# Optimization experiments

Measured on AMD Instinct MI355X. Metric: run time of the kernel, lower is better.

## Reference

```python
import jax, jax.numpy as jnp
import numpy as np

EPS = 1e-08


def setup_inputs() -> dict:
    key = jax.random.key(0)
    B, D = 8192, 512
    student_output = jax.random.normal(key, (B, D), dtype=jnp.float32)
    return {"student_output": student_output}


def reference(student_output) -> jnp.ndarray:
    # F.normalize(p=2, dim=-1, eps=EPS): x / max(||x||, eps)
    norm = jnp.linalg.norm(student_output, axis=-1, keepdims=True)
    x = student_output / jnp.maximum(norm, EPS)

    n = x.shape[0]
    # Pairwise inner products; mask the diagonal with -1 (self-match)
    dots = jnp.matmul(x, x.T)  # [B, B]
    idx = jnp.arange(n)
    dots = dots.at[idx, idx].set(-1.0)
    I = jnp.argmax(dots, axis=1)  # nearest neighbor index per row

    # torch.nn.PairwiseDistance(2, eps): ||x1 - x2 + eps||_2
    diff = x - x[I] + EPS
    distances = jnp.linalg.norm(diff, axis=-1)  # [B]
    loss = -jnp.mean(jnp.log(distances + EPS))
    return loss
```

## Files before the change

### kernel.cpp

```cpp
#include <hip/hip_runtime.h>
#include <hip/hip_bf16.h>
#include <math.h>

#define D_DIM 512
#define TM    128
#define TN    256

typedef int i32x4 __attribute__((ext_vector_type(4)));
typedef unsigned long long u64;


__device__ inline void async16(unsigned char* lds, const unsigned char* g) {
    __builtin_amdgcn_global_load_lds(
        (const __attribute__((address_space(1))) void*)g,
        (__attribute__((address_space(3))) void*)lds,
        16, 0, 0);
}


__global__ __launch_bounds__(256) void normalize_rows(
        const float* __restrict__ in, unsigned char* __restrict__ xb,
        float* __restrict__ inv_norm, u64* __restrict__ best,
        float* __restrict__ acc, int* __restrict__ cnt) {
    const int row  = blockIdx.x * 4 + (threadIdx.x >> 6);
    const int lane = threadIdx.x & 63;
    if (blockIdx.x == 0 && threadIdx.x == 0) { acc[0] = 0.f; cnt[0] = 0; }
    const float4* rp = (const float4*)(in + (size_t)row * D_DIM) + lane * 2;
    float4 a = rp[0], b = rp[1];
    float s = a.x*a.x + a.y*a.y + a.z*a.z + a.w*a.w
            + b.x*b.x + b.y*b.y + b.z*b.z + b.w*b.w;
    #pragma unroll
    for (int m = 1; m <= 32; m <<= 1) s += __shfl_xor(s, m, 64);
    float inv = 1.0f / fmaxf(sqrtf(s), 1e-8f);
    if (lane == 0) {
        inv_norm[row] = inv;
        best[row] = 0ull;
    }
    float sc = inv * 127.0f;
    int q0 = __float2int_rn(a.x*sc), q1 = __float2int_rn(a.y*sc);
    int q2 = __float2int_rn(a.z*sc), q3 = __float2int_rn(a.w*sc);
    int q4 = __float2int_rn(b.x*sc), q5 = __float2int_rn(b.y*sc);
    int q6 = __float2int_rn(b.z*sc), q7 = __float2int_rn(b.w*sc);
    int lo = (q0 & 255) | ((q1 & 255) << 8) | ((q2 & 255) << 16) | ((q3 & 255) << 24);
    int hi = (q4 & 255) | ((q5 & 255) << 8) | ((q6 & 255) << 16) | ((q7 & 255) << 24);
    ((int2*)(xb + (size_t)row * D_DIM))[lane] = make_int2(lo, hi);
}


__global__ __launch_bounds__(512, 4) void gemm_argmax(
        const unsigned char* __restrict__ X, u64* __restrict__ best) {
    __shared__ unsigned char smem[49152];
    unsigned char* As0 = smem;
    unsigned char* Bs0 = smem + 16384;
    unsigned int* rmerge = (unsigned int*)smem;
    unsigned int* cmerge = (unsigned int*)(smem + 2048);

    int l = blockIdx.x;
    int q = (int)(sqrtf((float)l / 16.0f + 0.25f) - 0.5f);
    while (16 * (q + 1) * (q + 2) <= l) ++q;
    while (16 * q * (q + 1) > l) --q;
    int rrem = l - 16 * q * (q + 1);
    int cw   = 8 * (q + 1);
    int c    = rrem / cw;
    int bi   = rrem - c * cw;
    int bj   = 4 * q + c;
    if (bi > 2 * bj + 1) return;
    const int m0 = bi * TM;
    const int n0 = bj * TN;

    const int t    = threadIdx.x;
    const int lane = t & 63;
    const int w    = t >> 6;
    const int wm   = w >> 2;
    const int wn   = w & 3;
    const int qr   = lane & 15;
    const int quad = lane >> 4;

    const int srcsl = ((t & 3) ^ ((t >> 3) & 3)) * 16;
    const unsigned char* gA  = X + (size_t)(m0 + (t >> 2)) * D_DIM + srcsl;
    const unsigned char* gB  = X + (size_t)(n0 + (t >> 2)) * D_DIM + srcsl;
    const unsigned char* gB2 = gB + (size_t)128 * D_DIM;

    #define STAGE(buf, k0)                                        \
        do {                                                      \
            async16(As0 + (buf) * 8192 + t * 16, gA + (k0));      \
            async16(Bs0 + (buf) * 16384 + t * 16, gB + (k0));     \
            async16(Bs0 + (buf) * 16384 + 8192 + t * 16, gB2 + (k0)); \
        } while (0)

    i32x4 accm[4][4];
    #pragma unroll
    for (int mi = 0; mi < 4; mi++)
        #pragma unroll
        for (int ni = 0; ni < 4; ni++)
            accm[mi][ni] = (i32x4){0, 0, 0, 0};

    const int rdsl = (quad ^ ((qr >> 1) & 3)) * 16;

    STAGE(0, 0);
    #pragma unroll
    for (int t8 = 0; t8 < 8; t8++) {
        const int cur = t8 & 1;
        if (t8 < 7) {
            STAGE(cur ^ 1, (t8 + 1) * 64);
            asm volatile("s_waitcnt vmcnt(3)" ::: "memory");
        } else {
            asm volatile("s_waitcnt vmcnt(0)" ::: "memory");
        }
        __builtin_amdgcn_s_barrier();

        i32x4 av[4], bv[4];
        const unsigned char* pA = As0 + cur * 8192  + (wm * 64 + qr) * 64 + rdsl;
        const unsigned char* pB = Bs0 + cur * 16384 + (wn * 64 + qr) * 64 + rdsl;
        #pragma unroll
        for (int mi = 0; mi < 4; mi++)
            av[mi] = *(const i32x4*)(pA + mi * 1024);
        #pragma unroll
        for (int ni = 0; ni < 4; ni++)
            bv[ni] = *(const i32x4*)(pB + ni * 1024);
        #pragma unroll
        for (int mi = 0; mi < 4; mi++)
            #pragma unroll
            for (int ni = 0; ni < 4; ni++)
                accm[mi][ni] = __builtin_amdgcn_mfma_i32_16x16x64_i8(
                    av[mi], bv[ni], accm[mi][ni], 0, 0, 0);

        asm volatile("" ::: "memory");
        __builtin_amdgcn_s_barrier();
    }
    #undef STAGE

    const int colg_base = n0 + wn * 64 + qr;

    #pragma unroll
    for (int mi = 0; mi < 4; mi++) {
        #pragma unroll
        for (int r = 0; r < 4; r++) {
            const int rowl = wm * 64 + mi * 16 + quad * 4 + r;
            const int rowg = m0 + rowl;
            unsigned key = 0u;
            #pragma unroll
            for (int ni = 0; ni < 4; ni++) {
                const int colg = colg_base + ni * 16;
                const unsigned lcol = (unsigned)(wn * 64 + ni * 16 + qr);
                unsigned k = (((unsigned)accm[mi][ni][r] + 0x800000u) << 8)
                           | (255u - lcol);
                k = (colg == rowg) ? 0u : k;
                key = key > k ? key : k;
            }
            #pragma unroll
            for (int m = 1; m <= 8; m <<= 1) {
                unsigned o = (unsigned)__shfl_xor((int)key, m, 64);
                key = key > o ? key : o;
            }
            if (qr == 0) rmerge[rowl * 4 + wn] = key;
        }
    }

    #pragma unroll
    for (int ni = 0; ni < 4; ni++) {
        const int colg = colg_base + ni * 16;
        unsigned key = 0u;
        #pragma unroll
        for (int mi = 0; mi < 4; mi++) {
            #pragma unroll
            for (int r = 0; r < 4; r++) {
                const unsigned lrow = (unsigned)(wm * 64 + mi * 16 + quad * 4 + r);
                const int rowg = m0 + (int)lrow;
                unsigned k = (((unsigned)accm[mi][ni][r] + 0x800000u) << 8)
                           | (255u - lrow);
                k = (rowg == colg) ? 0u : k;
                key = key > k ? key : k;
            }
        }
        unsigned o = (unsigned)__shfl_xor((int)key, 16, 64);
        key = key > o ? key : o;
        o = (unsigned)__shfl_xor((int)key, 32, 64);
        key = key > o ? key : o;
        if (quad == 0) cmerge[(wn * 64 + ni * 16 + qr) * 2 + wm] = key;
    }
    __syncthreads();

    if (t < TM) {
        unsigned a0 = rmerge[t * 4], a1 = rmerge[t * 4 + 1];
        unsigned a2 = rmerge[t * 4 + 2], a3 = rmerge[t * 4 + 3];
        unsigned k01 = a0 > a1 ? a0 : a1;
        unsigned k23 = a2 > a3 ? a2 : a3;
        unsigned k = k01 > k23 ? k01 : k23;
        unsigned bd32 = (k >> 8) + 0x7F800000u;
        unsigned colg = (unsigned)(n0 + 255) - (k & 255u);
        u64 kk = ((u64)bd32 << 32) | (u64)(0xFFFFFFFFu - colg);
        atomicMax(&best[m0 + t], kk);
    }
    if (t < TN) {
        unsigned c0 = cmerge[t * 2], c1 = cmerge[t * 2 + 1];
        unsigned k = c0 > c1 ? c0 : c1;
        unsigned bd32 = (k >> 8) + 0x7F800000u;
        unsigned rowg = (unsigned)(m0 + 255) - (k & 255u);
        u64 kk = ((u64)bd32 << 32) | (u64)(0xFFFFFFFFu - rowg);
        atomicMax(&best[n0 + t], kk);
    }
}


__global__ __launch_bounds__(256) void neighbor_reduce(
        const float* __restrict__ in, const float* __restrict__ inv_norm,
        const u64* __restrict__ best, float* __restrict__ acc,
        int* __restrict__ cnt, float* __restrict__ out, int B) {
    const int wave = threadIdx.x >> 6;
    const int lane = threadIdx.x & 63;
    float lsum = 0.f;
    #pragma unroll
    for (int rr = 0; rr < 8; rr++) {
        const int row = blockIdx.x * 32 + wave * 8 + rr;
        u64 k   = best[row];
        int nbr = (int)(0xFFFFFFFFu - (unsigned)(k & 0xFFFFFFFFull));
        float ir  = inv_norm[row];
        float inb = inv_norm[nbr];
        const float4* rp = (const float4*)(in + (size_t)row * D_DIM) + lane * 2;
        const float4* np = (const float4*)(in + (size_t)nbr * D_DIM) + lane * 2;
        float4 r0 = rp[0], r1 = rp[1], q0 = np[0], q1 = np[1];
        float d0 = r0.x*ir - q0.x*inb + 1e-8f, d1 = r0.y*ir - q0.y*inb + 1e-8f;
        float d2 = r0.z*ir - q0.z*inb + 1e-8f, d3 = r0.w*ir - q0.w*inb + 1e-8f;
        float d4 = r1.x*ir - q1.x*inb + 1e-8f, d5 = r1.y*ir - q1.y*inb + 1e-8f;
        float d6 = r1.z*ir - q1.z*inb + 1e-8f, d7 = r1.w*ir - q1.w*inb + 1e-8f;
        float s = d0*d0 + d1*d1 + d2*d2 + d3*d3 + d4*d4 + d5*d5 + d6*d6 + d7*d7;
        #pragma unroll
        for (int m = 1; m <= 32; m <<= 1) s += __shfl_xor(s, m, 64);
        if (lane == 0) lsum += logf(sqrtf(s) + 1e-8f);
    }
    __shared__ float sb[4];
    if (lane == 0) sb[wave] = lsum;
    __syncthreads();
    if (threadIdx.x == 0) {
        float partial = sb[0] + sb[1] + sb[2] + sb[3];
        atomicAdd(acc, partial);
        __threadfence();
        int done = atomicAdd(cnt, 1);
        if (done == gridDim.x - 1) {
            __threadfence();
            float tot = atomicAdd(acc, 0.0f);
            out[0] = -tot / (float)B;
        }
    }
}


extern "C" void kernel_launch(void* const* d_in, const int* in_sizes, int n_in,
                              void* d_out, int out_size, void* d_ws, size_t ws_size,
                              hipStream_t stream) {
    const float* in = (const float*)d_in[0];
    const int B = in_sizes[0] / D_DIM;
    const int nblk = 16 * 8 * 9;

    char* w = (char*)d_ws;
    unsigned char* xb = (unsigned char*)w;
    float* invn = (float*)(w + (size_t)B * D_DIM);
    u64*   best = (u64*)(w + (size_t)B * D_DIM + (size_t)B * 4);
    float* acc  = (float*)(w + (size_t)B * D_DIM + (size_t)B * 4 + (size_t)B * 8);
    int*   cnt  = (int*)(acc + 1);
    float* out  = (float*)d_out;

    normalize_rows<<<B / 4, 256, 0, stream>>>(in, xb, invn, best, acc, cnt);
    gemm_argmax<<<nblk, 512, 0, stream>>>(xb, best);
    neighbor_reduce<<<B / 32, 256, 0, stream>>>(in, invn, best, acc, cnt, out, B);
}
```

Measured before the change: 109.3 us.

## Switch int8 GEMM-argmax to square 128x128 triangular tiles with single-buffered K=128 stages

Replaces the 128x256 tile with 512 threads and double-buffered 64-wide K stages with a 128x128 tile using 256 threads. Each K stage is now 128 wide, loaded with a wider XOR swizzle and separated by __syncthreads, and the upper-triangular block enumeration is simplified. The aim is smaller blocks, more of them for better load balance, and fewer barriers per tile. The cost is losing the overlap between global loads and MFMA compute, plus lower operand reuse per block.

```diff
diff --git a/kernel.cpp b/kernel.cpp
--- a/kernel.cpp
+++ b/kernel.cpp
@@ -3,8 +3,7 @@
 #include <math.h>
 
 #define D_DIM 512
-#define TM    128
-#define TN    256
+#define TB    128
 
 typedef int i32x4 __attribute__((ext_vector_type(4)));
 typedef unsigned long long u64;
@@ -47,45 +46,44 @@
 }
 
 
-__global__ __launch_bounds__(512, 4) void gemm_argmax(
+__global__ __launch_bounds__(256, 4) void gemm_argmax(
         const unsigned char* __restrict__ X, u64* __restrict__ best) {
-    __shared__ unsigned char smem[49152];
-    unsigned char* As0 = smem;
-    unsigned char* Bs0 = smem + 16384;
+    __shared__ unsigned char smem[32768];
+    unsigned char* As = smem;
+    unsigned char* Bs = smem + 16384;
     unsigned int* rmerge = (unsigned int*)smem;
-    unsigned int* cmerge = (unsigned int*)(smem + 2048);
+    unsigned int* cmerge = (unsigned int*)(smem + 1024);
 
     int l = blockIdx.x;
-    int q = (int)(sqrtf((float)l / 16.0f + 0.25f) - 0.5f);
-    while (16 * (q + 1) * (q + 2) <= l) ++q;
-    while (16 * q * (q + 1) > l) --q;
-    int rrem = l - 16 * q * (q + 1);
-    int cw   = 8 * (q + 1);
-    int c    = rrem / cw;
-    int bi   = rrem - c * cw;
-    int bj   = 4 * q + c;
-    if (bi > 2 * bj + 1) return;
-    const int m0 = bi * TM;
-    const int n0 = bj * TN;
+    int bj = (int)((sqrtf(8.0f * (float)l + 1.0f) - 1.0f) * 0.5f);
+    while ((bj + 1) * (bj + 2) / 2 <= l) ++bj;
+    while (bj * (bj + 1) / 2 > l) --bj;
+    int bi = l - bj * (bj + 1) / 2;
+    const int m0 = bi * TB;
+    const int n0 = bj * TB;
 
     const int t    = threadIdx.x;
     const int lane = t & 63;
     const int w    = t >> 6;
-    const int wm   = w >> 2;
-    const int wn   = w & 3;
+    const int wm   = w >> 1;
+    const int wn   = w & 1;
     const int qr   = lane & 15;
     const int quad = lane >> 4;
 
-    const int srcsl = ((t & 3) ^ ((t >> 3) & 3)) * 16;
-    const unsigned char* gA  = X + (size_t)(m0 + (t >> 2)) * D_DIM + srcsl;
-    const unsigned char* gB  = X + (size_t)(n0 + (t >> 2)) * D_DIM + srcsl;
-    const unsigned char* gB2 = gB + (size_t)128 * D_DIM;
-
-    #define STAGE(buf, k0)                                        \
-        do {                                                      \
-            async16(As0 + (buf) * 8192 + t * 16, gA + (k0));      \
-            async16(Bs0 + (buf) * 16384 + t * 16, gB + (k0));     \
-            async16(Bs0 + (buf) * 16384 + 8192 + t * 16, gB2 + (k0)); \
+    const int srcsl = ((t & 7) ^ ((t >> 3) & 7)) * 16;
+    const unsigned char* gA = X + (size_t)(m0 + (t >> 3)) * D_DIM + srcsl;
+    const unsigned char* gB = X + (size_t)(n0 + (t >> 3)) * D_DIM + srcsl;
+
+    #define STAGE(k0)                                                   \
+        do {                                                            \
+            _Pragma("unroll")                                           \
+            for (int j = 0; j < 4; j++)                                 \
+                async16(As + j * 4096 + t * 16,                         \
+                        gA + (size_t)(j * 32) * D_DIM + (k0));          \
+            _Pragma("unroll")                                           \
+            for (int j = 0; j < 4; j++)                                 \
+                async16(Bs + j * 4096 + t * 16,                         \
+                        gB + (size_t)(j * 32) * D_DIM + (k0));          \
         } while (0)
 
     i32x4 accm[4][4];
@@ -95,38 +93,30 @@
         for (int ni = 0; ni < 4; ni++)
             accm[mi][ni] = (i32x4){0, 0, 0, 0};
 
-    const int rdsl = (quad ^ ((qr >> 1) & 3)) * 16;
-
-    STAGE(0, 0);
-    #pragma unroll
-    for (int t8 = 0; t8 < 8; t8++) {
-        const int cur = t8 & 1;
-        if (t8 < 7) {
-            STAGE(cur ^ 1, (t8 + 1) * 64);
-            asm volatile("s_waitcnt vmcnt(3)" ::: "memory");
-        } else {
-            asm volatile("s_waitcnt vmcnt(0)" ::: "memory");
-        }
-        __builtin_amdgcn_s_barrier();
-
-        i32x4 av[4], bv[4];
-        const unsigned char* pA = As0 + cur * 8192  + (wm * 64 + qr) * 64 + rdsl;
-        const unsigned char* pB = Bs0 + cur * 16384 + (wn * 64 + qr) * 64 + rdsl;
-        #pragma unroll
-        for (int mi = 0; mi < 4; mi++)
-            av[mi] = *(const i32x4*)(pA + mi * 1024);
-        #pragma unroll
-        for (int ni = 0; ni < 4; ni++)
-            bv[ni] = *(const i32x4*)(pB + ni * 1024);
-        #pragma unroll
-        for (int mi = 0; mi < 4; mi++)
+    #pragma unroll
+    for (int kt = 0; kt < 4; kt++) {
+        STAGE(kt * 128);
+        __syncthreads();
+        #pragma unroll
+        for (int ks = 0; ks < 2; ks++) {
+            const int pos = ((ks * 4 + quad) ^ (qr & 7)) * 16;
+            const unsigned char* pA = As + (wm * 64 + qr) * 128 + pos;
+            const unsigned char* pB = Bs + (wn * 64 + qr) * 128 + pos;
+            i32x4 av[4], bv[4];
+            #pragma unroll
+            for (int mi = 0; mi < 4; mi++)
+                av[mi] = *(const i32x4*)(pA + mi * 2048);
             #pragma unroll
             for (int ni = 0; ni < 4; ni++)
-                accm[mi][ni] = __builtin_amdgcn_mfma_i32_16x16x64_i8(
-                    av[mi], bv[ni], accm[mi][ni], 0, 0, 0);
-
-        asm volatile("" ::: "memory");
-        __builtin_amdgcn_s_barrier();
+                bv[ni] = *(const i32x4*)(pB + ni * 2048);
+            #pragma unroll
+            for (int mi = 0; mi < 4; mi++)
+                #pragma unroll
+                for (int ni = 0; ni < 4; ni++)
+                    accm[mi][ni] = __builtin_amdgcn_mfma_i32_16x16x64_i8(
+                        av[mi], bv[ni], accm[mi][ni], 0, 0, 0);
+        }
+        __syncthreads();
     }
     #undef STAGE
 
@@ -153,7 +143,7 @@
                 unsigned o = (unsigned)__shfl_xor((int)key, m, 64);
                 key = key > o ? key : o;
             }
-            if (qr == 0) rmerge[rowl * 4 + wn] = key;
+            if (qr == 0) rmerge[rowl * 2 + wn] = key;
         }
     }
 
@@ -181,24 +171,21 @@
     }
     __syncthreads();
 
-    if (t < TM) {
-        unsigned a0 = rmerge[t * 4], a1 = rmerge[t * 4 + 1];
-        unsigned a2 = rmerge[t * 4 + 2], a3 = rmerge[t * 4 + 3];
-        unsigned k01 = a0 > a1 ? a0 : a1;
-        unsigned k23 = a2 > a3 ? a2 : a3;
-        unsigned k = k01 > k23 ? k01 : k23;
+    if (t < TB) {
+        unsigned a0 = rmerge[t * 2], a1 = rmerge[t * 2 + 1];
+        unsigned k = a0 > a1 ? a0 : a1;
         unsigned bd32 = (k >> 8) + 0x7F800000u;
         unsigned colg = (unsigned)(n0 + 255) - (k & 255u);
         u64 kk = ((u64)bd32 << 32) | (u64)(0xFFFFFFFFu - colg);
         atomicMax(&best[m0 + t], kk);
-    }
-    if (t < TN) {
-        unsigned c0 = cmerge[t * 2], c1 = cmerge[t * 2 + 1];
+    } else {
+        const int tt = t - TB;
+        unsigned c0 = cmerge[tt * 2], c1 = cmerge[tt * 2 + 1];
         unsigned k = c0 > c1 ? c0 : c1;
         unsigned bd32 = (k >> 8) + 0x7F800000u;
         unsigned rowg = (unsigned)(m0 + 255) - (k & 255u);
         u64 kk = ((u64)bd32 << 32) | (u64)(0xFFFFFFFFu - rowg);
-        atomicMax(&best[n0 + t], kk);
+        atomicMax(&best[n0 + tt], kk);
     }
 }
 
@@ -251,7 +238,8 @@
                               hipStream_t stream) {
     const float* in = (const float*)d_in[0];
     const int B = in_sizes[0] / D_DIM;
-    const int nblk = 16 * 8 * 9;
+    const int nb = B / TB;
+    const int nblk = nb * (nb + 1) / 2;
 
     char* w = (char*)d_ws;
     unsigned char* xb = (unsigned char*)w;
@@ -262,6 +250,6 @@
     float* out  = (float*)d_out;
 
     normalize_rows<<<B / 4, 256, 0, stream>>>(in, xb, invn, best, acc, cnt);
-    gemm_argmax<<<nblk, 512, 0, stream>>>(xb, best);
+    gemm_argmax<<<nblk, 256, 0, stream>>>(xb, best);
     neighbor_reduce<<<B / 32, 256, 0, stream>>>(in, invn, best, acc, cnt, out, B);
 }
```

Result: slower. 115.2 us (+5.5%).
